# Kernel optimization log

Measured on AMD Instinct MI355X. Metric: run time of the kernel, lower is better.

The kernel has to match this reference:

```python
import jax, jax.numpy as jnp
import numpy as np

DMODEL = 512
NUM_HEADS = 8
HEAD_DIM = DMODEL // NUM_HEADS


def setup_inputs() -> dict:
    key = jax.random.key(0)
    k1, k2, k3, k4, k5 = jax.random.split(key, 5)
    x = jax.random.normal(k1, (4, 2048, DMODEL), dtype=jnp.float32)
    s = 1.0 / np.sqrt(DMODEL)
    W_qkv = jax.random.uniform(k2, (DMODEL, 3 * DMODEL), jnp.float32, -s, s)
    b_qkv = jax.random.uniform(k3, (3 * DMODEL,), jnp.float32, -s, s)
    W_out = jax.random.uniform(k4, (DMODEL, DMODEL), jnp.float32, -s, s)
    b_out = jax.random.uniform(k5, (DMODEL,), jnp.float32, -s, s)
    return {"x": x, "W_qkv": W_qkv, "b_qkv": b_qkv, "W_out": W_out, "b_out": b_out}


def reference(x, W_qkv, b_qkv, W_out, b_out):
    B, T, D = x.shape
    H, Hd = NUM_HEADS, HEAD_DIM
    qkv = x @ W_qkv + b_qkv                      # [B, T, 3D]
    qkv = qkv.reshape(B, T, 3, H, Hd).transpose(2, 0, 3, 1, 4)  # [3, B, H, T, Hd]
    q, k, v = qkv[0], qkv[1], qkv[2]
    scores = jnp.einsum('bhqd,bhkd->bhqk', q, k) / np.sqrt(Hd)  # [B, H, T, T]
    causal = jnp.tril(jnp.ones((T, T), dtype=bool))
    scores = jnp.where(causal, scores, -jnp.inf)
    weights = jax.nn.softmax(scores, axis=-1)
    out = jnp.einsum('bhqk,bhkd->bhqd', weights, v)  # [B, H, T, Hd]
    out = out.transpose(0, 2, 1, 3).reshape(B, T, D)
    return out @ W_out + b_out
```

## Files before the change

kernel.cpp:

```cpp
#include <hip/hip_runtime.h>
#include <cstdint>
#include <cstddef>

#define D_MODEL 512
#define SEQ_T 2048
#define NHEADS 8
#define HDIM 64

typedef __attribute__((ext_vector_type(8))) short bf16x8;
typedef __attribute__((ext_vector_type(4))) float f32x4;

__device__ __forceinline__ unsigned short f2bf(float f) {
  unsigned int u = __float_as_uint(f);
  u += 0x7FFFu + ((u >> 16) & 1u);
  return (unsigned short)(u >> 16);
}

__device__ __forceinline__ unsigned int pack_bf16(float lo, float hi) {
  unsigned int a = __float_as_uint(lo) + 0x8000u;
  unsigned int b = __float_as_uint(hi) + 0x8000u;
  return __builtin_amdgcn_perm(b, a, 0x07060302u);
}

#define QSCALE 0.18033688011112043f
#define SSHIFT 16.0f

__device__ __forceinline__ void async_lds16(const unsigned short* g,
                                            unsigned short* l) {
  __builtin_amdgcn_global_load_lds(
      (const __attribute__((address_space(1))) void*)g,
      (__attribute__((address_space(3))) void*)l, 16, 0, 0);
}

__global__ __launch_bounds__(256) void prep_kernel(
    const float* __restrict__ x, const float* __restrict__ W_qkv,
    const float* __restrict__ W_out, unsigned short* __restrict__ xb,
    unsigned short* __restrict__ Wqkt, unsigned short* __restrict__ Wot) {
  __shared__ float tile[64][65];
  const int bid = blockIdx.x;
  if (bid < 2048) {
    int i = (bid * 256 + threadIdx.x) * 8;
    float4 a = *(const float4*)(x + i);
    float4 b = *(const float4*)(x + i + 4);
    ushort4 lo = {f2bf(a.x), f2bf(a.y), f2bf(a.z), f2bf(a.w)};
    ushort4 hi = {f2bf(b.x), f2bf(b.y), f2bf(b.z), f2bf(b.w)};
    *(ushort4*)(xb + i) = lo;
    *(ushort4*)(xb + i + 4) = hi;
    return;
  }
  const float* src;
  unsigned short* dst;
  int R = 512, C, c0, r0;
  if (bid < 2048 + 192) {
    int t = bid - 2048;
    C = 1536; c0 = (t % 24) * 64; r0 = (t / 24) * 64;
    src = W_qkv; dst = Wqkt;
  } else {
    int t = bid - 2240;
    C = 512; c0 = (t & 7) * 64; r0 = (t >> 3) * 64;
    src = W_out; dst = Wot;
  }
  for (int i = threadIdx.x; i < 64 * 64; i += 256) {
    int r = i >> 6, c = i & 63;
    tile[r][c] = src[(size_t)(r0 + r) * C + c0 + c];
  }
  __syncthreads();
  for (int i = threadIdx.x; i < 64 * 64; i += 256) {
    int c = i >> 6, r = i & 63;
    dst[(size_t)(c0 + c) * R + r0 + r] = f2bf(tile[r][c]);
  }
}

__global__ __launch_bounds__(256) void gemm_qkv_mfma(
    const unsigned short* __restrict__ xb, const unsigned short* __restrict__ Wt,
    const float* __restrict__ bias, unsigned short* __restrict__ Qtb,
    unsigned short* __restrict__ Kb, unsigned short* __restrict__ Vtb) {
  __shared__ unsigned short As[128 * 64];
  __shared__ unsigned short Bs[128 * 64];
  const int tid = threadIdx.x;
  const int w = tid >> 6, lane = tid & 63;
  const int quad = lane >> 4, l15 = lane & 15;
  const int wm = w >> 1, wn = w & 1;
  const int m0 = blockIdx.x * 128, n0 = blockIdx.y * 128;

  const int srow = tid >> 3;
  const int schunk = (tid & 7) ^ (srow & 7);
  const unsigned short* ga = xb + (size_t)(m0 + srow) * 512 + schunk * 8;
  const unsigned short* gb = Wt + (size_t)(n0 + srow) * 512 + schunk * 8;
  unsigned short* lA = As + tid * 8;
  unsigned short* lB = Bs + tid * 8;

  f32x4 acc[4][4] = {};
  for (int k0 = 0; k0 < 512; k0 += 64) {
#pragma unroll
    for (int rr = 0; rr < 4; ++rr) {
      async_lds16(ga + (size_t)rr * 32 * 512 + k0, lA + rr * 2048);
      async_lds16(gb + (size_t)rr * 32 * 512 + k0, lB + rr * 2048);
    }
    __syncthreads();
    bf16x8 af[4][2], bfr[4][2];
#pragma unroll
    for (int mb = 0; mb < 4; ++mb) {
      int row = wm * 64 + mb * 16 + l15;
#pragma unroll
      for (int kk = 0; kk < 2; ++kk) {
        int slot = (kk * 4 + quad) ^ (row & 7);
        af[mb][kk] = *(const bf16x8*)&As[row * 64 + slot * 8];
      }
    }
#pragma unroll
    for (int nb = 0; nb < 4; ++nb) {
      int row = wn * 64 + nb * 16 + l15;
#pragma unroll
      for (int kk = 0; kk < 2; ++kk) {
        int slot = (kk * 4 + quad) ^ (row & 7);
        bfr[nb][kk] = *(const bf16x8*)&Bs[row * 64 + slot * 8];
      }
    }
#pragma unroll
    for (int mb = 0; mb < 4; ++mb)
#pragma unroll
      for (int nb = 0; nb < 4; ++nb) {
        acc[mb][nb] = __builtin_amdgcn_mfma_f32_16x16x32_bf16(
            af[mb][0], bfr[nb][0], acc[mb][nb], 0, 0, 0);
        acc[mb][nb] = __builtin_amdgcn_mfma_f32_16x16x32_bf16(
            af[mb][1], bfr[nb][1], acc[mb][nb], 0, 0, 0);
      }
    __syncthreads();
  }

  const int cbase = n0 + wn * 64;
  const int three = cbase >> 9;
  const int h = (cbase >> 6) & 7;
  const int bh = ((m0 >> 11) << 3) + h;
  const int t0 = (m0 & 2047) + wm * 64;
  float bv[4];
#pragma unroll
  for (int nb = 0; nb < 4; ++nb) bv[nb] = bias[cbase + nb * 16 + l15];

  if (three == 0) {
#pragma unroll
    for (int mb = 0; mb < 4; ++mb)
#pragma unroll
      for (int nb = 0; nb < 4; ++nb) {
        int trow = t0 + mb * 16 + quad * 4;
        ushort4 v = {f2bf((acc[mb][nb][0] + bv[nb]) * QSCALE),
                     f2bf((acc[mb][nb][1] + bv[nb]) * QSCALE),
                     f2bf((acc[mb][nb][2] + bv[nb]) * QSCALE),
                     f2bf((acc[mb][nb][3] + bv[nb]) * QSCALE)};
        *(ushort4*)(Qtb + ((size_t)bh * HDIM + nb * 16 + l15) * SEQ_T + trow) = v;
      }
  } else if (three == 2) {
#pragma unroll
    for (int mb = 0; mb < 4; ++mb)
#pragma unroll
      for (int nb = 0; nb < 4; ++nb) {
        int trow = t0 + mb * 16 + quad * 4;
        ushort4 v = {f2bf(acc[mb][nb][0] + bv[nb]), f2bf(acc[mb][nb][1] + bv[nb]),
                     f2bf(acc[mb][nb][2] + bv[nb]), f2bf(acc[mb][nb][3] + bv[nb])};
        *(ushort4*)(Vtb + ((size_t)bh * HDIM + nb * 16 + l15) * SEQ_T + trow) = v;
      }
  } else {
#pragma unroll
    for (int mb = 0; mb < 4; ++mb)
#pragma unroll
      for (int nb = 0; nb < 4; ++nb)
#pragma unroll
        for (int r = 0; r < 4; ++r) {
          int trow = t0 + mb * 16 + quad * 4 + r;
          Kb[((size_t)bh * SEQ_T + trow) * HDIM + nb * 16 + l15] =
              f2bf(acc[mb][nb][r] + bv[nb]);
        }
  }
}

__global__ __launch_bounds__(256, 4) void attn_mfma5(
    const unsigned short* __restrict__ Qtb, const unsigned short* __restrict__ Kb,
    const unsigned short* __restrict__ Vtb, unsigned short* __restrict__ AOb) {
  __shared__ __align__(16) unsigned short Ks[2][64 * 64];
  __shared__ __align__(16) unsigned short Vs[2][64 * 64];
  __shared__ __align__(16) unsigned short Pt[4][16 * 64];
  const int tid = threadIdx.x;
  const int w = tid >> 6, lane = tid & 63;
  const int quad = lane >> 4, l15 = lane & 15;

  const int bid = blockIdx.x;
  const int xcd = bid & 7;
  const int j = bid >> 3;
  const int c = j & 31, g = j >> 5;
  const int k = c >> 2;
  const int bh = xcd + 8 * (c & 3);
  const int qt = (g == 0) ? (31 - k) : (g == 1) ? (16 + k)
               : (g == 2) ? (15 - k) : k;

  const unsigned short* kbase = Kb + (size_t)bh * SEQ_T * HDIM;
  const unsigned short* vbase = Vtb + (size_t)bh * HDIM * SEQ_T;
  const int sr = tid >> 3;
  const int lc = tid & 7;
  const int scol = lc * 8;
  const int swc = (lc ^ (sr & 7)) * 8;

  bf16x8 qf0, qf1;
  {
    unsigned short qraw[16];
    const unsigned short* qp =
        Qtb + ((size_t)bh * HDIM + quad * 8) * SEQ_T + qt * 64 + w * 16 + l15;
#pragma unroll
    for (int jj = 0; jj < 8; ++jj) {
      qraw[jj] = qp[(size_t)jj * SEQ_T];
      qraw[8 + jj] = qp[(size_t)(32 + jj) * SEQ_T];
    }
    qf0 = *(const bf16x8*)qraw;
    qf1 = *(const bf16x8*)(qraw + 8);
  }
  const short oneb = (short)0x3F80;
  const bf16x8 ones = {oneb, oneb, oneb, oneb, oneb, oneb, oneb, oneb};

  f32x4 O[4] = {{0.f, 0.f, 0.f, 0.f}, {0.f, 0.f, 0.f, 0.f},
                {0.f, 0.f, 0.f, 0.f}, {0.f, 0.f, 0.f, 0.f}};
  f32x4 l_acc = {0.f, 0.f, 0.f, 0.f};
  const int q_rel = w * 16 + l15;
  const int r7 = l15 & 7;

  uint4 rk0, rk1, rv0, rv1;
  {
    const unsigned short* kp = kbase + (size_t)sr * 64 + scol;
    rk0 = *(const uint4*)kp;
    rk1 = *(const uint4*)(kp + 32 * 64);
    const unsigned short* vp = vbase + (size_t)sr * SEQ_T + scol;
    rv0 = *(const uint4*)vp;
    rv1 = *(const uint4*)(vp + 32 * SEQ_T);
  }
  *(uint4*)&Ks[0][sr * 64 + swc] = rk0;
  *(uint4*)&Ks[0][(sr + 32) * 64 + swc] = rk1;
  *(uint4*)&Vs[0][sr * 64 + swc] = rv0;
  *(uint4*)&Vs[0][(sr + 32) * 64 + swc] = rv1;
  __syncthreads();

  for (int i = 0; i < qt; ++i) {
    const int cur = i & 1;
    {
      const int nkt = i + 1;
      const unsigned short* kp = kbase + (size_t)(nkt * 64 + sr) * 64 + scol;
      rk0 = *(const uint4*)kp;
      rk1 = *(const uint4*)(kp + 32 * 64);
      const unsigned short* vp = vbase + (size_t)sr * SEQ_T + nkt * 64 + scol;
      rv0 = *(const uint4*)vp;
      rv1 = *(const uint4*)(vp + 32 * SEQ_T);
    }

    f32x4 S[4];
#pragma unroll
    for (int nb = 0; nb < 4; ++nb) {
      const int row = nb * 16 + l15;
      const unsigned short* k0p = &Ks[cur][row * 64 + ((quad ^ r7) * 8)];
      const unsigned short* k1p = &Ks[cur][row * 64 + (((quad + 4) ^ r7) * 8)];
      f32x4 z = {0.f, 0.f, 0.f, 0.f};
      z = __builtin_amdgcn_mfma_f32_16x16x32_bf16(*(const bf16x8*)k0p, qf0, z,
                                                  0, 0, 0);
      S[nb] = __builtin_amdgcn_mfma_f32_16x16x32_bf16(*(const bf16x8*)k1p, qf1,
                                                      z, 0, 0, 0);
    }

#pragma unroll
    for (int nb = 0; nb < 4; ++nb) {
      float p0 = __builtin_amdgcn_exp2f(S[nb][0] - SSHIFT);
      float p1 = __builtin_amdgcn_exp2f(S[nb][1] - SSHIFT);
      float p2 = __builtin_amdgcn_exp2f(S[nb][2] - SSHIFT);
      float p3 = __builtin_amdgcn_exp2f(S[nb][3] - SSHIFT);
      int cc = 2 * nb + (quad >> 1);
      uint2 pk = {pack_bf16(p0, p1), pack_bf16(p2, p3)};
      *(uint2*)&Pt[w][l15 * 64 + ((cc ^ r7) * 8) + (quad & 1) * 4] = pk;
    }

    bf16x8 pb0 = *(const bf16x8*)&Pt[w][l15 * 64 + ((quad ^ r7) * 8)];
    bf16x8 pb1 = *(const bf16x8*)&Pt[w][l15 * 64 + (((quad + 4) ^ r7) * 8)];
    l_acc = __builtin_amdgcn_mfma_f32_16x16x32_bf16(ones, pb0, l_acc, 0, 0, 0);
    l_acc = __builtin_amdgcn_mfma_f32_16x16x32_bf16(ones, pb1, l_acc, 0, 0, 0);
#pragma unroll
    for (int nbd = 0; nbd < 4; ++nbd) {
      const int row = nbd * 16 + l15;
      const unsigned short* v0p = &Vs[cur][row * 64 + ((quad ^ r7) * 8)];
      const unsigned short* v1p = &Vs[cur][row * 64 + (((quad + 4) ^ r7) * 8)];
      O[nbd] = __builtin_amdgcn_mfma_f32_16x16x32_bf16(*(const bf16x8*)v0p, pb0,
                                                       O[nbd], 0, 0, 0);
      O[nbd] = __builtin_amdgcn_mfma_f32_16x16x32_bf16(*(const bf16x8*)v1p, pb1,
                                                       O[nbd], 0, 0, 0);
    }

    const int nxt = cur ^ 1;
    *(uint4*)&Ks[nxt][sr * 64 + swc] = rk0;
    *(uint4*)&Ks[nxt][(sr + 32) * 64 + swc] = rk1;
    *(uint4*)&Vs[nxt][sr * 64 + swc] = rv0;
    *(uint4*)&Vs[nxt][(sr + 32) * 64 + swc] = rv1;
    __syncthreads();
  }

  {
    const int cur = qt & 1;
    const int nb_lim = w + 1;
    f32x4 S[4];
#pragma unroll
    for (int nb = 0; nb < 4; ++nb) {
      if (nb < nb_lim) {
        const int row = nb * 16 + l15;
        const unsigned short* k0p = &Ks[cur][row * 64 + ((quad ^ r7) * 8)];
        const unsigned short* k1p =
            &Ks[cur][row * 64 + (((quad + 4) ^ r7) * 8)];
        f32x4 z = {0.f, 0.f, 0.f, 0.f};
        z = __builtin_amdgcn_mfma_f32_16x16x32_bf16(*(const bf16x8*)k0p, qf0,
                                                    z, 0, 0, 0);
        S[nb] = __builtin_amdgcn_mfma_f32_16x16x32_bf16(*(const bf16x8*)k1p,
                                                        qf1, z, 0, 0, 0);
      }
    }
#pragma unroll
    for (int nb = 0; nb < 4; ++nb) {
      int cc = 2 * nb + (quad >> 1);
      if (nb < nb_lim) {
        float pp[4];
#pragma unroll
        for (int r = 0; r < 4; ++r) {
          float p = __builtin_amdgcn_exp2f(S[nb][r] - SSHIFT);
          int key_rel = nb * 16 + quad * 4 + r;
          pp[r] = (key_rel > q_rel) ? 0.f : p;
        }
        uint2 pk = {pack_bf16(pp[0], pp[1]), pack_bf16(pp[2], pp[3])};
        *(uint2*)&Pt[w][l15 * 64 + ((cc ^ r7) * 8) + (quad & 1) * 4] = pk;
      } else {
        uint2 z2 = {0u, 0u};
        *(uint2*)&Pt[w][l15 * 64 + ((cc ^ r7) * 8) + (quad & 1) * 4] = z2;
      }
    }
    const int kpv = (w >= 2) ? 2 : 1;
    bf16x8 pb0 = *(const bf16x8*)&Pt[w][l15 * 64 + ((quad ^ r7) * 8)];
    bf16x8 pb1 = *(const bf16x8*)&Pt[w][l15 * 64 + (((quad + 4) ^ r7) * 8)];
    l_acc = __builtin_amdgcn_mfma_f32_16x16x32_bf16(ones, pb0, l_acc, 0, 0, 0);
    if (kpv == 2)
      l_acc =
          __builtin_amdgcn_mfma_f32_16x16x32_bf16(ones, pb1, l_acc, 0, 0, 0);
#pragma unroll
    for (int nbd = 0; nbd < 4; ++nbd) {
      const int row = nbd * 16 + l15;
      const unsigned short* v0p = &Vs[cur][row * 64 + ((quad ^ r7) * 8)];
      O[nbd] = __builtin_amdgcn_mfma_f32_16x16x32_bf16(*(const bf16x8*)v0p, pb0,
                                                       O[nbd], 0, 0, 0);
      if (kpv == 2) {
        const unsigned short* v1p =
            &Vs[cur][row * 64 + (((quad + 4) ^ r7) * 8)];
        O[nbd] = __builtin_amdgcn_mfma_f32_16x16x32_bf16(*(const bf16x8*)v1p,
                                                         pb1, O[nbd], 0, 0, 0);
      }
    }
  }

  float inv = 1.0f / l_acc[0];
  const int bb = bh >> 3, h = bh & 7;
  int qrow = qt * 64 + q_rel;
  unsigned short* dst = AOb + ((size_t)bb * SEQ_T + qrow) * D_MODEL + (h << 6);
#pragma unroll
  for (int nbd = 0; nbd < 4; ++nbd) {
    ushort4 o4 = {f2bf(O[nbd][0] * inv), f2bf(O[nbd][1] * inv),
                  f2bf(O[nbd][2] * inv), f2bf(O[nbd][3] * inv)};
    *(ushort4*)(dst + nbd * 16 + quad * 4) = o4;
  }
}

__global__ __launch_bounds__(256) void gemm_out_mfma(
    const unsigned short* __restrict__ AOb, const unsigned short* __restrict__ Wot,
    const float* __restrict__ bias, float* __restrict__ out) {
  __shared__ unsigned short As[64 * 64];
  __shared__ unsigned short Bs[128 * 64];
  const int tid = threadIdx.x;
  const int w = tid >> 6, lane = tid & 63;
  const int quad = lane >> 4, l15 = lane & 15;
  const int m0 = blockIdx.x * 64, n0 = blockIdx.y * 128;

  const int srow = tid >> 3;
  const int schunk = (tid & 7) ^ (srow & 7);
  const unsigned short* ga = AOb + (size_t)(m0 + srow) * 512 + schunk * 8;
  const unsigned short* gb = Wot + (size_t)(n0 + srow) * 512 + schunk * 8;
  unsigned short* lA = As + tid * 8;
  unsigned short* lB = Bs + tid * 8;

  f32x4 acc[4][2] = {};
  for (int k0 = 0; k0 < 512; k0 += 64) {
#pragma unroll
    for (int rr = 0; rr < 2; ++rr)
      async_lds16(ga + (size_t)rr * 32 * 512 + k0, lA + rr * 2048);
#pragma unroll
    for (int rr = 0; rr < 4; ++rr)
      async_lds16(gb + (size_t)rr * 32 * 512 + k0, lB + rr * 2048);
    __syncthreads();
    bf16x8 af[4][2], bfr[2][2];
#pragma unroll
    for (int mb = 0; mb < 4; ++mb) {
      int row = mb * 16 + l15;
#pragma unroll
      for (int kk = 0; kk < 2; ++kk) {
        int slot = (kk * 4 + quad) ^ (row & 7);
        af[mb][kk] = *(const bf16x8*)&As[row * 64 + slot * 8];
      }
    }
#pragma unroll
    for (int nb = 0; nb < 2; ++nb) {
      int row = w * 32 + nb * 16 + l15;
#pragma unroll
      for (int kk = 0; kk < 2; ++kk) {
        int slot = (kk * 4 + quad) ^ (row & 7);
        bfr[nb][kk] = *(const bf16x8*)&Bs[row * 64 + slot * 8];
      }
    }
#pragma unroll
    for (int mb = 0; mb < 4; ++mb)
#pragma unroll
      for (int nb = 0; nb < 2; ++nb) {
        acc[mb][nb] = __builtin_amdgcn_mfma_f32_16x16x32_bf16(
            af[mb][0], bfr[nb][0], acc[mb][nb], 0, 0, 0);
        acc[mb][nb] = __builtin_amdgcn_mfma_f32_16x16x32_bf16(
            af[mb][1], bfr[nb][1], acc[mb][nb], 0, 0, 0);
      }
    __syncthreads();
  }

  const int cbase = n0 + w * 32;
  float bv[2];
#pragma unroll
  for (int nb = 0; nb < 2; ++nb) bv[nb] = bias[cbase + nb * 16 + l15];
#pragma unroll
  for (int mb = 0; mb < 4; ++mb)
#pragma unroll
    for (int nb = 0; nb < 2; ++nb)
#pragma unroll
      for (int r = 0; r < 4; ++r)
        out[(size_t)(m0 + mb * 16 + quad * 4 + r) * 512 + cbase + nb * 16 +
            l15] = acc[mb][nb][r] + bv[nb];
}

extern "C" void kernel_launch(void* const* d_in, const int* in_sizes, int n_in,
                              void* d_out, int out_size, void* d_ws,
                              size_t ws_size, hipStream_t stream) {
  const float* x     = (const float*)d_in[0];
  const float* W_qkv = (const float*)d_in[1];
  const float* b_qkv = (const float*)d_in[2];
  const float* W_out = (const float*)d_in[3];
  const float* b_out = (const float*)d_in[4];
  float* out = (float*)d_out;

  const size_t NX = (size_t)4 * SEQ_T * D_MODEL;
  unsigned short* xb   = (unsigned short*)d_ws;
  unsigned short* Wqkt = xb + NX;
  unsigned short* Wot  = Wqkt + (size_t)1536 * 512;
  unsigned short* Qtb  = Wot + (size_t)512 * 512;
  unsigned short* Kb   = Qtb + NX;
  unsigned short* Vtb  = Kb + NX;
  unsigned short* AOb  = Vtb + NX;

  prep_kernel<<<2304, 256, 0, stream>>>(x, W_qkv, W_out, xb, Wqkt, Wot);
  gemm_qkv_mfma<<<dim3(64, 12), 256, 0, stream>>>(xb, Wqkt, b_qkv, Qtb, Kb,
                                                  Vtb);
  attn_mfma5<<<dim3(1024), 256, 0, stream>>>(Qtb, Kb, Vtb, AOb);
  gemm_out_mfma<<<dim3(128, 4), 256, 0, stream>>>(AOb, Wot, b_out, out);
}
```

Baseline: 132.7 us.

## Rewrite attention with 32x32 MFMA and 128-row query tiles per block

The attention kernel now gives each wave 32 query rows (128 per block) and uses 32x32x16 bf16 MFMA for both QK^T and PV. Halving the block count doubles how many queries reuse each K/V tile staged in LDS. The row-sum moves from an MFMA against a ones vector to scalar adds plus a shuffle, and the causal diagonal is handled by two masked tiles. In exchange, register pressure rises (launch bounds drop to 2 blocks), the grid is only 512 blocks with a coarser load-balancing scheme, and waves in the lower half of the block sit idle during the final tile.

```diff
diff --git a/kernel.cpp b/kernel.cpp
--- a/kernel.cpp
+++ b/kernel.cpp
@@ -9,6 +9,7 @@
 
 typedef __attribute__((ext_vector_type(8))) short bf16x8;
 typedef __attribute__((ext_vector_type(4))) float f32x4;
+typedef __attribute__((ext_vector_type(16))) float f32x16;
 
 __device__ __forceinline__ unsigned short f2bf(float f) {
   unsigned int u = __float_as_uint(f);
@@ -174,24 +175,25 @@
   }
 }
 
-__global__ __launch_bounds__(256, 4) void attn_mfma5(
+__global__ __launch_bounds__(256, 2) void attn_mfma6(
     const unsigned short* __restrict__ Qtb, const unsigned short* __restrict__ Kb,
     const unsigned short* __restrict__ Vtb, unsigned short* __restrict__ AOb) {
   __shared__ __align__(16) unsigned short Ks[2][64 * 64];
   __shared__ __align__(16) unsigned short Vs[2][64 * 64];
-  __shared__ __align__(16) unsigned short Pt[4][16 * 64];
+  __shared__ __align__(16) unsigned short Pt[4][32 * 64];
   const int tid = threadIdx.x;
   const int w = tid >> 6, lane = tid & 63;
-  const int quad = lane >> 4, l15 = lane & 15;
+  const int l31 = lane & 31, h = lane >> 5;
+  const int r7l = lane & 7;
 
   const int bid = blockIdx.x;
   const int xcd = bid & 7;
   const int j = bid >> 3;
   const int c = j & 31, g = j >> 5;
-  const int k = c >> 2;
+  const int kslot = c >> 2;
   const int bh = xcd + 8 * (c & 3);
-  const int qt = (g == 0) ? (31 - k) : (g == 1) ? (16 + k)
-               : (g == 2) ? (15 - k) : k;
+  const int qt2 = g ? kslot : (15 - kslot);
+  const int nmain = 2 * qt2;
 
   const unsigned short* kbase = Kb + (size_t)bh * SEQ_T * HDIM;
   const unsigned short* vbase = Vtb + (size_t)bh * HDIM * SEQ_T;
@@ -200,45 +202,88 @@
   const int scol = lc * 8;
   const int swc = (lc ^ (sr & 7)) * 8;
 
-  bf16x8 qf0, qf1;
+  const int qglob = qt2 * 128 + w * 32 + l31;
+  bf16x8 qf[4];
   {
-    unsigned short qraw[16];
+    unsigned short qraw[32];
     const unsigned short* qp =
-        Qtb + ((size_t)bh * HDIM + quad * 8) * SEQ_T + qt * 64 + w * 16 + l15;
-#pragma unroll
-    for (int jj = 0; jj < 8; ++jj) {
-      qraw[jj] = qp[(size_t)jj * SEQ_T];
-      qraw[8 + jj] = qp[(size_t)(32 + jj) * SEQ_T];
-    }
-    qf0 = *(const bf16x8*)qraw;
-    qf1 = *(const bf16x8*)(qraw + 8);
-  }
-  const short oneb = (short)0x3F80;
-  const bf16x8 ones = {oneb, oneb, oneb, oneb, oneb, oneb, oneb, oneb};
-
-  f32x4 O[4] = {{0.f, 0.f, 0.f, 0.f}, {0.f, 0.f, 0.f, 0.f},
-                {0.f, 0.f, 0.f, 0.f}, {0.f, 0.f, 0.f, 0.f}};
-  f32x4 l_acc = {0.f, 0.f, 0.f, 0.f};
-  const int q_rel = w * 16 + l15;
-  const int r7 = l15 & 7;
-
-  uint4 rk0, rk1, rv0, rv1;
+        Qtb + ((size_t)bh * HDIM + h * 8) * SEQ_T + qglob;
+#pragma unroll
+    for (int cc = 0; cc < 4; ++cc)
+#pragma unroll
+      for (int jj = 0; jj < 8; ++jj)
+        qraw[cc * 8 + jj] = qp[(size_t)(cc * 16 + jj) * SEQ_T];
+#pragma unroll
+    for (int cc = 0; cc < 4; ++cc) qf[cc] = *(const bf16x8*)(qraw + cc * 8);
+  }
+
+  f32x16 O0 = {0.f, 0.f, 0.f, 0.f, 0.f, 0.f, 0.f, 0.f,
+               0.f, 0.f, 0.f, 0.f, 0.f, 0.f, 0.f, 0.f};
+  f32x16 O1 = O0;
+  float l_acc = 0.f;
+
+  auto tile_compute = [&](int cur, int lim, bool masked) {
+    f32x16 S0 = {0.f, 0.f, 0.f, 0.f, 0.f, 0.f, 0.f, 0.f,
+                 0.f, 0.f, 0.f, 0.f, 0.f, 0.f, 0.f, 0.f};
+    f32x16 S1 = S0;
+#pragma unroll
+    for (int cc = 0; cc < 4; ++cc) {
+      const int slot = ((cc << 1) | h) ^ r7l;
+      const bf16x8 k0 = *(const bf16x8*)&Ks[cur][l31 * 64 + slot * 8];
+      const bf16x8 k1 = *(const bf16x8*)&Ks[cur][(32 + l31) * 64 + slot * 8];
+      S0 = __builtin_amdgcn_mfma_f32_32x32x16_bf16(k0, qf[cc], S0, 0, 0, 0);
+      S1 = __builtin_amdgcn_mfma_f32_32x32x16_bf16(k1, qf[cc], S1, 0, 0, 0);
+    }
+#pragma unroll
+    for (int m = 0; m < 8; ++m) {
+      float p0 = __builtin_amdgcn_exp2f(S0[2 * m] - SSHIFT);
+      float p1 = __builtin_amdgcn_exp2f(S0[2 * m + 1] - SSHIFT);
+      float p2 = __builtin_amdgcn_exp2f(S1[2 * m] - SSHIFT);
+      float p3 = __builtin_amdgcn_exp2f(S1[2 * m + 1] - SSHIFT);
+      if (masked) {
+        const int r0 = 2 * m, r1 = 2 * m + 1;
+        const int kl0 = (r0 & 3) + 8 * (r0 >> 2) + 4 * h;
+        const int kl1 = (r1 & 3) + 8 * (r1 >> 2) + 4 * h;
+        p0 = (kl0 > lim) ? 0.f : p0;
+        p1 = (kl1 > lim) ? 0.f : p1;
+        p2 = (kl0 + 32 > lim) ? 0.f : p2;
+        p3 = (kl1 + 32 > lim) ? 0.f : p3;
+      }
+      l_acc += (p0 + p1) + (p2 + p3);
+      const int within = 2 * (m & 1) + 4 * h;
+      const int slot0 = (m >> 1) ^ r7l;
+      const int slot1 = ((m >> 1) + 4) ^ r7l;
+      *(unsigned int*)&Pt[w][l31 * 64 + slot0 * 8 + within] = pack_bf16(p0, p1);
+      *(unsigned int*)&Pt[w][l31 * 64 + slot1 * 8 + within] = pack_bf16(p2, p3);
+    }
+#pragma unroll
+    for (int t = 0; t < 4; ++t) {
+      const int slot = ((t << 1) | h) ^ r7l;
+      const bf16x8 pb = *(const bf16x8*)&Pt[w][l31 * 64 + slot * 8];
+      const bf16x8 v0 = *(const bf16x8*)&Vs[cur][l31 * 64 + slot * 8];
+      const bf16x8 v1 = *(const bf16x8*)&Vs[cur][(32 + l31) * 64 + slot * 8];
+      O0 = __builtin_amdgcn_mfma_f32_32x32x16_bf16(v0, pb, O0, 0, 0, 0);
+      O1 = __builtin_amdgcn_mfma_f32_32x32x16_bf16(v1, pb, O1, 0, 0, 0);
+    }
+  };
+
   {
     const unsigned short* kp = kbase + (size_t)sr * 64 + scol;
-    rk0 = *(const uint4*)kp;
-    rk1 = *(const uint4*)(kp + 32 * 64);
+    uint4 rk0 = *(const uint4*)kp;
+    uint4 rk1 = *(const uint4*)(kp + 32 * 64);
     const unsigned short* vp = vbase + (size_t)sr * SEQ_T + scol;
-    rv0 = *(const uint4*)vp;
-    rv1 = *(const uint4*)(vp + 32 * SEQ_T);
-  }
-  *(uint4*)&Ks[0][sr * 64 + swc] = rk0;
-  *(uint4*)&Ks[0][(sr + 32) * 64 + swc] = rk1;
-  *(uint4*)&Vs[0][sr * 64 + swc] = rv0;
-  *(uint4*)&Vs[0][(sr + 32) * 64 + swc] = rv1;
+    uint4 rv0 = *(const uint4*)vp;
+    uint4 rv1 = *(const uint4*)(vp + 32 * SEQ_T);
+    *(uint4*)&Ks[0][sr * 64 + swc] = rk0;
+    *(uint4*)&Ks[0][(sr + 32) * 64 + swc] = rk1;
+    *(uint4*)&Vs[0][sr * 64 + swc] = rv0;
+    *(uint4*)&Vs[0][(sr + 32) * 64 + swc] = rv1;
+  }
   __syncthreads();
 
-  for (int i = 0; i < qt; ++i) {
+  for (int i = 0; i < nmain; ++i) {
     const int cur = i & 1;
+    uint4 rk0, rk1, rv0, rv1;
     {
       const int nkt = i + 1;
       const unsigned short* kp = kbase + (size_t)(nkt * 64 + sr) * 64 + scol;
@@ -248,46 +293,7 @@
       rv0 = *(const uint4*)vp;
       rv1 = *(const uint4*)(vp + 32 * SEQ_T);
     }
-
-    f32x4 S[4];
-#pragma unroll
-    for (int nb = 0; nb < 4; ++nb) {
-      const int row = nb * 16 + l15;
-      const unsigned short* k0p = &Ks[cur][row * 64 + ((quad ^ r7) * 8)];
-      const unsigned short* k1p = &Ks[cur][row * 64 + (((quad + 4) ^ r7) * 8)];
-      f32x4 z = {0.f, 0.f, 0.f, 0.f};
-      z = __builtin_amdgcn_mfma_f32_16x16x32_bf16(*(const bf16x8*)k0p, qf0, z,
-                                                  0, 0, 0);
-      S[nb] = __builtin_amdgcn_mfma_f32_16x16x32_bf16(*(const bf16x8*)k1p, qf1,
-                                                      z, 0, 0, 0);
-    }
-
-#pragma unroll
-    for (int nb = 0; nb < 4; ++nb) {
-      float p0 = __builtin_amdgcn_exp2f(S[nb][0] - SSHIFT);
-      float p1 = __builtin_amdgcn_exp2f(S[nb][1] - SSHIFT);
-      float p2 = __builtin_amdgcn_exp2f(S[nb][2] - SSHIFT);
-      float p3 = __builtin_amdgcn_exp2f(S[nb][3] - SSHIFT);
-      int cc = 2 * nb + (quad >> 1);
-      uint2 pk = {pack_bf16(p0, p1), pack_bf16(p2, p3)};
-      *(uint2*)&Pt[w][l15 * 64 + ((cc ^ r7) * 8) + (quad & 1) * 4] = pk;
-    }
-
-    bf16x8 pb0 = *(const bf16x8*)&Pt[w][l15 * 64 + ((quad ^ r7) * 8)];
-    bf16x8 pb1 = *(const bf16x8*)&Pt[w][l15 * 64 + (((quad + 4) ^ r7) * 8)];
-    l_acc = __builtin_amdgcn_mfma_f32_16x16x32_bf16(ones, pb0, l_acc, 0, 0, 0);
-    l_acc = __builtin_amdgcn_mfma_f32_16x16x32_bf16(ones, pb1, l_acc, 0, 0, 0);
-#pragma unroll
-    for (int nbd = 0; nbd < 4; ++nbd) {
-      const int row = nbd * 16 + l15;
-      const unsigned short* v0p = &Vs[cur][row * 64 + ((quad ^ r7) * 8)];
-      const unsigned short* v1p = &Vs[cur][row * 64 + (((quad + 4) ^ r7) * 8)];
-      O[nbd] = __builtin_amdgcn_mfma_f32_16x16x32_bf16(*(const bf16x8*)v0p, pb0,
-                                                       O[nbd], 0, 0, 0);
-      O[nbd] = __builtin_amdgcn_mfma_f32_16x16x32_bf16(*(const bf16x8*)v1p, pb1,
-                                                       O[nbd], 0, 0, 0);
-    }
-
+    tile_compute(cur, 0, false);
     const int nxt = cur ^ 1;
     *(uint4*)&Ks[nxt][sr * 64 + swc] = rk0;
     *(uint4*)&Ks[nxt][(sr + 32) * 64 + swc] = rk1;
@@ -297,72 +303,40 @@
   }
 
   {
-    const int cur = qt & 1;
-    const int nb_lim = w + 1;
-    f32x4 S[4];
-#pragma unroll
-    for (int nb = 0; nb < 4; ++nb) {
-      if (nb < nb_lim) {
-        const int row = nb * 16 + l15;
-        const unsigned short* k0p = &Ks[cur][row * 64 + ((quad ^ r7) * 8)];
-        const unsigned short* k1p =
-            &Ks[cur][row * 64 + (((quad + 4) ^ r7) * 8)];
-        f32x4 z = {0.f, 0.f, 0.f, 0.f};
-        z = __builtin_amdgcn_mfma_f32_16x16x32_bf16(*(const bf16x8*)k0p, qf0,
-                                                    z, 0, 0, 0);
-        S[nb] = __builtin_amdgcn_mfma_f32_16x16x32_bf16(*(const bf16x8*)k1p,
-                                                        qf1, z, 0, 0, 0);
-      }
-    }
-#pragma unroll
-    for (int nb = 0; nb < 4; ++nb) {
-      int cc = 2 * nb + (quad >> 1);
-      if (nb < nb_lim) {
-        float pp[4];
-#pragma unroll
-        for (int r = 0; r < 4; ++r) {
-          float p = __builtin_amdgcn_exp2f(S[nb][r] - SSHIFT);
-          int key_rel = nb * 16 + quad * 4 + r;
-          pp[r] = (key_rel > q_rel) ? 0.f : p;
-        }
-        uint2 pk = {pack_bf16(pp[0], pp[1]), pack_bf16(pp[2], pp[3])};
-        *(uint2*)&Pt[w][l15 * 64 + ((cc ^ r7) * 8) + (quad & 1) * 4] = pk;
-      } else {
-        uint2 z2 = {0u, 0u};
-        *(uint2*)&Pt[w][l15 * 64 + ((cc ^ r7) * 8) + (quad & 1) * 4] = z2;
-      }
-    }
-    const int kpv = (w >= 2) ? 2 : 1;
-    bf16x8 pb0 = *(const bf16x8*)&Pt[w][l15 * 64 + ((quad ^ r7) * 8)];
-    bf16x8 pb1 = *(const bf16x8*)&Pt[w][l15 * 64 + (((quad + 4) ^ r7) * 8)];
-    l_acc = __builtin_amdgcn_mfma_f32_16x16x32_bf16(ones, pb0, l_acc, 0, 0, 0);
-    if (kpv == 2)
-      l_acc =
-          __builtin_amdgcn_mfma_f32_16x16x32_bf16(ones, pb1, l_acc, 0, 0, 0);
-#pragma unroll
-    for (int nbd = 0; nbd < 4; ++nbd) {
-      const int row = nbd * 16 + l15;
-      const unsigned short* v0p = &Vs[cur][row * 64 + ((quad ^ r7) * 8)];
-      O[nbd] = __builtin_amdgcn_mfma_f32_16x16x32_bf16(*(const bf16x8*)v0p, pb0,
-                                                       O[nbd], 0, 0, 0);
-      if (kpv == 2) {
-        const unsigned short* v1p =
-            &Vs[cur][row * 64 + (((quad + 4) ^ r7) * 8)];
-        O[nbd] = __builtin_amdgcn_mfma_f32_16x16x32_bf16(*(const bf16x8*)v1p,
-                                                         pb1, O[nbd], 0, 0, 0);
-      }
-    }
-  }
-
-  float inv = 1.0f / l_acc[0];
-  const int bb = bh >> 3, h = bh & 7;
-  int qrow = qt * 64 + q_rel;
-  unsigned short* dst = AOb + ((size_t)bb * SEQ_T + qrow) * D_MODEL + (h << 6);
-#pragma unroll
-  for (int nbd = 0; nbd < 4; ++nbd) {
-    ushort4 o4 = {f2bf(O[nbd][0] * inv), f2bf(O[nbd][1] * inv),
-                  f2bf(O[nbd][2] * inv), f2bf(O[nbd][3] * inv)};
-    *(ushort4*)(dst + nbd * 16 + quad * 4) = o4;
+    const int cur = nmain & 1;
+    const int nkt = nmain + 1;
+    const unsigned short* kp = kbase + (size_t)(nkt * 64 + sr) * 64 + scol;
+    uint4 rk0 = *(const uint4*)kp;
+    uint4 rk1 = *(const uint4*)(kp + 32 * 64);
+    const unsigned short* vp = vbase + (size_t)sr * SEQ_T + nkt * 64 + scol;
+    uint4 rv0 = *(const uint4*)vp;
+    uint4 rv1 = *(const uint4*)(vp + 32 * SEQ_T);
+    tile_compute(cur, w * 32 + l31, true);
+    const int nxt = cur ^ 1;
+    *(uint4*)&Ks[nxt][sr * 64 + swc] = rk0;
+    *(uint4*)&Ks[nxt][(sr + 32) * 64 + swc] = rk1;
+    *(uint4*)&Vs[nxt][sr * 64 + swc] = rv0;
+    *(uint4*)&Vs[nxt][(sr + 32) * 64 + swc] = rv1;
+    __syncthreads();
+  }
+
+  if (w >= 2) {
+    const int cur = (nmain + 1) & 1;
+    tile_compute(cur, w * 32 + l31 - 64, true);
+  }
+
+  l_acc += __shfl_xor(l_acc, 32, 64);
+  const float inv = 1.0f / fmaxf(l_acc, 1e-30f);
+  const int bb = bh >> 3, hh = bh & 7;
+  unsigned short* dst = AOb + ((size_t)bb * SEQ_T + qglob) * D_MODEL + (hh << 6);
+#pragma unroll
+  for (int rg = 0; rg < 4; ++rg) {
+    ushort4 o0 = {f2bf(O0[4 * rg + 0] * inv), f2bf(O0[4 * rg + 1] * inv),
+                  f2bf(O0[4 * rg + 2] * inv), f2bf(O0[4 * rg + 3] * inv)};
+    *(ushort4*)(dst + 8 * rg + 4 * h) = o0;
+    ushort4 o1 = {f2bf(O1[4 * rg + 0] * inv), f2bf(O1[4 * rg + 1] * inv),
+                  f2bf(O1[4 * rg + 2] * inv), f2bf(O1[4 * rg + 3] * inv)};
+    *(ushort4*)(dst + 32 + 8 * rg + 4 * h) = o1;
   }
 }
 
@@ -459,6 +433,6 @@
   prep_kernel<<<2304, 256, 0, stream>>>(x, W_qkv, W_out, xb, Wqkt, Wot);
   gemm_qkv_mfma<<<dim3(64, 12), 256, 0, stream>>>(xb, Wqkt, b_qkv, Qtb, Kb,
                                                   Vtb);
-  attn_mfma5<<<dim3(1024), 256, 0, stream>>>(Qtb, Kb, Vtb, AOb);
+  attn_mfma6<<<dim3(512), 256, 0, stream>>>(Qtb, Kb, Vtb, AOb);
   gemm_out_mfma<<<dim3(128, 4), 256, 0, stream>>>(AOb, Wot, b_out, out);
 }
```

New measurement: 147.8 us. 1.11x slower.
